# Optimization experiments

Hardware: AMD Instinct MI355X
Metric: run time of the kernel (lower is better)

The kernel has to match this reference:

```python
import jax, jax.numpy as jnp
import numpy as np

B, N, F_IN, H, C = 32768, 12, 128, 4, 64  # batch, nodes/graph, input_dim, heads, hidden_dim
NEG_SLOPE = 0.2  # PyG GATConv default leaky_relu slope


def setup_inputs() -> dict:
    key = jax.random.key(0)
    ks = jax.random.split(key, 16)
    def xavier(k, shape):
        fan_in, fan_out = shape[0], int(np.prod(shape[1:]))
        lim = float(np.sqrt(6.0 / (fan_in + fan_out)))
        return jax.random.uniform(k, shape, jnp.float32, -lim, lim)
    return {
        "node_features": jax.random.normal(ks[0], (B, N, F_IN), jnp.float32),
        "W1": xavier(ks[1], (F_IN, H, C)),
        "a_src1": xavier(ks[2], (H, C)),
        "a_dst1": xavier(ks[3], (H, C)),
        "b1": jnp.zeros((H * C,), jnp.float32),
        "W2": xavier(ks[4], (H * C, 1, C)),
        "a_src2": xavier(ks[5], (1, C)),
        "a_dst2": xavier(ks[6], (1, C)),
        "b2": jnp.zeros((C,), jnp.float32),
        # classifier head: 64 -> 32 -> 1
        "Wc1": xavier(ks[7], (C, C // 2)),
        "bc1": jnp.zeros((C // 2,), jnp.float32),
        "Wc2": xavier(ks[8], (C // 2, 1)),
        "bc2": jnp.zeros((1,), jnp.float32),
    }


def gat_dense(x, W, a_src, a_dst, bias, concat):
    # x: [B, N, F].  Fully-connected graph + self-loops (PyG GATConv default)
    # == dense attention over all N nodes of each graph.
    h = jnp.einsum("bnf,fhc->bnhc", x, W)               # [B,N,H,C]
    e_src = jnp.einsum("bnhc,hc->bnh", h, a_src)         # alpha contrib of source j
    e_dst = jnp.einsum("bnhc,hc->bnh", h, a_dst)         # alpha contrib of target i
    # edge (j -> i): logit = leaky_relu(e_dst[i] + e_src[j])
    logits = jax.nn.leaky_relu(e_dst[:, :, None, :] + e_src[:, None, :, :], NEG_SLOPE)  # [B,i,j,H]
    alpha = jax.nn.softmax(logits, axis=2)               # softmax over neighbors j
    out = jnp.einsum("bijh,bjhc->bihc", alpha, h)        # aggregate
    if concat:
        out = out.reshape(out.shape[0], out.shape[1], -1)
    else:
        out = out.mean(axis=2)
    return out + bias


def reference(node_features, W1, a_src1, a_dst1, b1, W2, a_src2, a_dst2, b2,
              Wc1, bc1, Wc2, bc2):
    # eval mode: dropouts are identity; is_finetune=False so finetune_block skipped
    x = jax.nn.elu(gat_dense(node_features, W1, a_src1, a_dst1, b1, concat=True))   # [B,N,256]
    x = jax.nn.elu(gat_dense(x, W2, a_src2, a_dst2, b2, concat=False))              # [B,N,64]
    g = x.mean(axis=1)                                                              # global_mean_pool -> [B,64]
    hdn = jax.nn.relu(g @ Wc1 + bc1)
    logits = hdn @ Wc2 + bc2                                                        # [B,1]
    return logits
```

## Files before the change

kernel.cpp:

```cpp
#include <hip/hip_runtime.h>
#include <math.h>

typedef __attribute__((ext_vector_type(8))) short bf16x8;
typedef __attribute__((ext_vector_type(4))) float f32x4;

namespace {
constexpr int NN  = 12;
constexpr int FIN = 128;
constexpr int D1  = 256;
constexpr int C2  = 64;
constexpr float SLOPE = 0.2f;

__device__ __forceinline__ unsigned short f2bf(float f) {
    unsigned u = __builtin_bit_cast(unsigned, f);
    u += 0x7FFFu + ((u >> 16) & 1u);
    return (unsigned short)(u >> 16);
}
__device__ __forceinline__ unsigned pktrunc(float lo, float hi) {
    return __builtin_amdgcn_perm(__builtin_bit_cast(unsigned, hi),
                                 __builtin_bit_cast(unsigned, lo), 0x07060302u);
}
__device__ __forceinline__ float elu1(float x) { return x > 0.f ? x : __expf(x) - 1.f; }
__device__ __forceinline__ float lrelu(float x) { return x > 0.f ? x : SLOPE * x; }
}

__global__ void prep_weights(const float* __restrict__ W1, const float* __restrict__ as1,
                             const float* __restrict__ ad1,
                             const float* __restrict__ W2, const float* __restrict__ as2,
                             const float* __restrict__ ad2,
                             unsigned short* __restrict__ wsB1, unsigned short* __restrict__ wsB2) {
    int t = blockIdx.x * 256 + threadIdx.x;
    if (t < 34816) {
        int i = t & 7, l = (t >> 3) & 63, kn = t >> 9;
        int kt = kn / 17, nt = kn % 17;
        int k = kt * 32 + (l >> 4) * 8 + i;
        float v = 0.f;
        if (nt < 16) {
            v = W1[k * 256 + nt * 16 + (l & 15)];
        } else {
            int cc = l & 15;
            if (cc < 4)      for (int c = 0; c < 64; ++c) v += W1[k * 256 + cc * 64 + c] * as1[cc * 64 + c];
            else if (cc < 8) for (int c = 0; c < 64; ++c) v += W1[k * 256 + (cc - 4) * 64 + c] * ad1[(cc - 4) * 64 + c];
        }
        wsB1[t] = f2bf(v);
    } else if (t < 55296) {
        int t2 = t - 34816;
        int i = t2 & 7, l = (t2 >> 3) & 63, kn = t2 >> 9;
        int kt = kn / 5, nt = kn % 5;
        int k = kt * 32 + (l >> 4) * 8 + i;
        float v = 0.f;
        if (nt < 4) {
            v = W2[k * 64 + nt * 16 + (l & 15)];
        } else {
            int cc = l & 15;
            if (cc == 0)      for (int c = 0; c < 64; ++c) v += W2[k * 64 + c] * as2[c];
            else if (cc == 1) for (int c = 0; c < 64; ++c) v += W2[k * 64 + c] * ad2[c];
        }
        wsB2[t2] = f2bf(v);
    }
}

__global__ __launch_bounds__(512, 4) void gat_mfma8(
    const float* __restrict__ x_in,
    const unsigned short* __restrict__ wsB1,
    const unsigned short* __restrict__ wsB2,
    const float* __restrict__ b1, const float* __restrict__ b2,
    const float* __restrict__ Wc1, const float* __restrict__ bc1,
    const float* __restrict__ Wc2, const float* __restrict__ bc2,
    float* __restrict__ out)
{
    __shared__ __align__(16) unsigned char R0[13056];
    __shared__ __align__(16) unsigned char R1[32768];
    __shared__ __align__(16) unsigned char R2[24576];
    __shared__ float eS1[48][4], eD1[48][4];
    __shared__ float eS2[48], eD2[48];
    __shared__ float gpool[4][64];

    const int b = blockIdx.x, t = threadIdx.x;
    const int w = t >> 6, l = t & 63, l15 = l & 15, lq = l >> 4;

    {
        const float4* xs = (const float4*)(x_in + (size_t)b * (4 * NN * FIN));
        #pragma unroll
        for (int it = 0; it < 3; ++it) {
            int q = t + 512 * it;
            float4 v = xs[q];
            int e0 = q << 2, r = e0 >> 7, k = e0 & 127;
            int addr = ((r << 8) + (k << 1)) ^ ((r & 7) << 4);
            *(uint2*)(R0 + addr) = make_uint2(pktrunc(v.x, v.y), pktrunc(v.z, v.w));
        }
        #pragma unroll
        for (int it = 0; it < 3; ++it)
            *(uint4*)(R2 + ((it * 512 + t) << 4)) = make_uint4(0, 0, 0, 0);
        {
            int col = t >> 1, bs = 6 + (t & 1);
            int addr = ((col << 7) + (bs << 4)) ^ ((col & 7) << 4);
            *(uint4*)(R1 + addr) = make_uint4(0, 0, 0, 0);
        }
    }
    __syncthreads();

    {
        const uint4* pb = (const uint4*)wsB1;
        const int h = w >> 1, half = w & 1;
        bf16x8 Bf[2][4];
        #pragma unroll
        for (int ngl = 0; ngl < 2; ++ngl)
            #pragma unroll
            for (int kt = 0; kt < 4; ++kt)
                Bf[ngl][kt] = __builtin_bit_cast(bf16x8, pb[(kt * 17 + (h * 4 + half * 2 + ngl)) * 64 + l]);
        bf16x8 Bfe[4];
        if (w == 0) {
            #pragma unroll
            for (int kt = 0; kt < 4; ++kt)
                Bfe[kt] = __builtin_bit_cast(bf16x8, pb[(kt * 17 + 16) * 64 + l]);
        }
        #pragma unroll
        for (int m = 0; m < 3; ++m) {
            int r = m * 16 + l15, abase = (r << 8) + (lq << 4), swz = (r & 7) << 4;
            bf16x8 Af[4];
            #pragma unroll
            for (int kt = 0; kt < 4; ++kt)
                Af[kt] = *(const bf16x8*)(R0 + ((abase + (kt << 6)) ^ swz));
            f32x4 acc[2];
            #pragma unroll
            for (int ngl = 0; ngl < 2; ++ngl) acc[ngl] = (f32x4){0.f, 0.f, 0.f, 0.f};
            #pragma unroll
            for (int ngl = 0; ngl < 2; ++ngl)
                #pragma unroll
                for (int kt = 0; kt < 4; ++kt)
                    acc[ngl] = __builtin_amdgcn_mfma_f32_16x16x32_bf16(Af[kt], Bf[ngl][kt], acc[ngl], 0, 0, 0);
            int row0 = m * 16 + lq * 4;
            #pragma unroll
            for (int ngl = 0; ngl < 2; ++ngl) {
                int col = h * 64 + (half * 2 + ngl) * 16 + l15;
                int addr = ((col << 7) + (row0 << 1)) ^ ((col & 7) << 4);
                *(uint2*)(R1 + addr) = make_uint2(pktrunc(acc[ngl][0], acc[ngl][1]),
                                                  pktrunc(acc[ngl][2], acc[ngl][3]));
            }
            if (w == 0) {
                f32x4 acce = (f32x4){0.f, 0.f, 0.f, 0.f};
                #pragma unroll
                for (int kt = 0; kt < 4; ++kt)
                    acce = __builtin_amdgcn_mfma_f32_16x16x32_bf16(Af[kt], Bfe[kt], acce, 0, 0, 0);
                if (l15 < 8) {
                    #pragma unroll
                    for (int reg = 0; reg < 4; ++reg) {
                        int row = row0 + reg;
                        if (l15 < 4) eS1[row][l15] = acce[reg];
                        else         eD1[row][l15 - 4] = acce[reg];
                    }
                }
            }
        }
    }
    __syncthreads();

    if (t < 192) {
        int g = t / 48, rem = t % 48, i = rem >> 2, h = rem & 3;
        int rowi = g * 12 + i;
        float edi = eD1[rowi][h];
        float lv[12]; float mx = -1e30f;
        #pragma unroll
        for (int j = 0; j < 12; ++j) {
            float v = lrelu(edi + eS1[g * 12 + j][h]);
            lv[j] = v; mx = fmaxf(mx, v);
        }
        float s = 0.f;
        #pragma unroll
        for (int j = 0; j < 12; ++j) { lv[j] = __expf(lv[j] - mx); s += lv[j]; }
        float inv = 1.f / s;
        unsigned char* base = R2 + h * 6144;
        int rb = rowi << 7, swz = (rowi & 7) << 4, ob = g * 24;
        #pragma unroll
        for (int p = 0; p < 3; ++p) {
            unsigned q0 = (unsigned)f2bf(lv[4*p]   * inv) | ((unsigned)f2bf(lv[4*p+1] * inv) << 16);
            unsigned q1 = (unsigned)f2bf(lv[4*p+2] * inv) | ((unsigned)f2bf(lv[4*p+3] * inv) << 16);
            int addr = (rb + ob + p * 8) ^ swz;
            *(uint2*)(base + addr) = make_uint2(q0, q1);
        }
    }
    __syncthreads();

    {
        const int h = w >> 1, half = w & 1;
        bf16x8 Ba[3][2];
        const unsigned char* ab = R2 + h * 6144;
        #pragma unroll
        for (int nt = 0; nt < 3; ++nt)
            #pragma unroll
            for (int kt = 0; kt < 2; ++kt) {
                int i = nt * 16 + l15;
                Ba[nt][kt] = *(const bf16x8*)(ab + (((i << 7) + (kt << 6) + (lq << 4)) ^ ((i & 7) << 4)));
            }
        __syncthreads();
        #pragma unroll
        for (int mtl = 0; mtl < 2; ++mtl) {
            int mt = half * 2 + mtl;
            int o = h * 64 + mt * 16 + l15;
            bf16x8 Ah[2];
            #pragma unroll
            for (int kt = 0; kt < 2; ++kt)
                Ah[kt] = *(const bf16x8*)(R1 + (((o << 7) + (kt << 6) + (lq << 4)) ^ ((o & 7) << 4)));
            int o0 = h * 64 + mt * 16 + (lq << 2);
            float4 b1v = *(const float4*)(b1 + o0);
            float bb[4] = {b1v.x, b1v.y, b1v.z, b1v.w};
            #pragma unroll
            for (int nt = 0; nt < 3; ++nt) {
                f32x4 acc = (f32x4){0.f, 0.f, 0.f, 0.f};
                #pragma unroll
                for (int kt = 0; kt < 2; ++kt)
                    acc = __builtin_amdgcn_mfma_f32_16x16x32_bf16(Ah[kt], Ba[nt][kt], acc, 0, 0, 0);
                float e0 = elu1(acc[0] + bb[0]), e1 = elu1(acc[1] + bb[1]);
                float e2 = elu1(acc[2] + bb[2]), e3 = elu1(acc[3] + bb[3]);
                int i = nt * 16 + l15;
                int addr = ((i << 9) + (o0 << 1)) ^ ((i & 7) << 4);
                *(uint2*)(R2 + addr) = make_uint2(pktrunc(e0, e1), pktrunc(e2, e3));
            }
        }
    }
    __syncthreads();

    {
        if (t < 128) {
            int col = t >> 1, bs = 6 + (t & 1);
            int addr = ((col << 7) + (bs << 4)) ^ ((col & 7) << 4);
            *(uint4*)(R1 + addr) = make_uint4(0, 0, 0, 0);
        }
        if (t < 192) {
            *(uint4*)(R1 + 8192 + (t << 4)) = make_uint4(0, 0, 0, 0);
            *(uint4*)(R1 + 8192 + ((t + 192) << 4)) = make_uint4(0, 0, 0, 0);
        }
        const uint4* pb2 = (const uint4*)wsB2;
        #pragma unroll
        for (int ui = 0; ui < 2; ++ui) {
            int u = w * 2 + ui;
            if (u < 15) {
                int tile = u / 3, m = u % 3;
                bf16x8 Bg[8];
                #pragma unroll
                for (int kt = 0; kt < 8; ++kt)
                    Bg[kt] = __builtin_bit_cast(bf16x8, pb2[(kt * 5 + tile) * 64 + l]);
                int r = m * 16 + l15, swz = (r & 7) << 4;
                f32x4 acc = (f32x4){0.f, 0.f, 0.f, 0.f};
                #pragma unroll
                for (int kt = 0; kt < 8; ++kt) {
                    int addr = ((r << 9) + (kt << 6) + (lq << 4)) ^ swz;
                    bf16x8 Ax = *(const bf16x8*)(R2 + addr);
                    acc = __builtin_amdgcn_mfma_f32_16x16x32_bf16(Ax, Bg[kt], acc, 0, 0, 0);
                }
                int row0 = m * 16 + lq * 4;
                if (tile < 4) {
                    int col = tile * 16 + l15;
                    int addr = ((col << 7) + (row0 << 1)) ^ ((col & 7) << 4);
                    *(uint2*)(R1 + addr) = make_uint2(pktrunc(acc[0], acc[1]),
                                                      pktrunc(acc[2], acc[3]));
                } else if (l15 < 2) {
                    #pragma unroll
                    for (int reg = 0; reg < 4; ++reg) {
                        int row = row0 + reg;
                        if (l15 == 0) eS2[row] = acc[reg];
                        else          eD2[row] = acc[reg];
                    }
                }
            }
        }
    }
    __syncthreads();

    if (t < 48) {
        int g = t / 12;
        float edi = eD2[t];
        float lv[12]; float mx = -1e30f;
        #pragma unroll
        for (int j = 0; j < 12; ++j) {
            float v = lrelu(edi + eS2[g * 12 + j]);
            lv[j] = v; mx = fmaxf(mx, v);
        }
        float s = 0.f;
        #pragma unroll
        for (int j = 0; j < 12; ++j) { lv[j] = __expf(lv[j] - mx); s += lv[j]; }
        float inv = 1.f / s;
        int rb = t << 7, swz = (t & 7) << 4, ob = g * 24;
        #pragma unroll
        for (int p = 0; p < 3; ++p) {
            unsigned q0 = (unsigned)f2bf(lv[4*p]   * inv) | ((unsigned)f2bf(lv[4*p+1] * inv) << 16);
            unsigned q1 = (unsigned)f2bf(lv[4*p+2] * inv) | ((unsigned)f2bf(lv[4*p+3] * inv) << 16);
            int addr = 8192 + ((rb + ob + p * 8) ^ swz);
            *(uint2*)(R1 + addr) = make_uint2(q0, q1);
        }
    }
    __syncthreads();

    {
        const int mt = w & 3;
        const int nt0 = (w < 4) ? 0 : 2;
        const int ntc = (w < 4) ? 2 : 1;
        int o = mt * 16 + l15;
        bf16x8 Ah2[2];
        #pragma unroll
        for (int kt = 0; kt < 2; ++kt)
            Ah2[kt] = *(const bf16x8*)(R1 + (((o << 7) + (kt << 6) + (lq << 4)) ^ ((o & 7) << 4)));
        int ost = mt * 16 + (lq << 2);
        float4 b2v = *(const float4*)(b2 + ost);
        float bb[4] = {b2v.x, b2v.y, b2v.z, b2v.w};
        for (int ni = 0; ni < ntc; ++ni) {
            int nt = nt0 + ni;
            int i = nt * 16 + l15;
            bf16x8 Ba2[2];
            #pragma unroll
            for (int kt = 0; kt < 2; ++kt)
                Ba2[kt] = *(const bf16x8*)(R1 + 8192 + (((i << 7) + (kt << 6) + (lq << 4)) ^ ((i & 7) << 4)));
            f32x4 acc = (f32x4){0.f, 0.f, 0.f, 0.f};
            #pragma unroll
            for (int kt = 0; kt < 2; ++kt)
                acc = __builtin_amdgcn_mfma_f32_16x16x32_bf16(Ah2[kt], Ba2[kt], acc, 0, 0, 0);
            #pragma unroll
            for (int reg = 0; reg < 4; ++reg)
                *(float*)(R0 + (ost + reg) * 200 + (i << 2)) = elu1(acc[reg] + bb[reg]);
        }
    }
    __syncthreads();

    if (t < 256) {
        int o = t & 63, g = t >> 6;
        const unsigned char* row = R0 + o * 200 + g * 48;
        float s = 0.f;
        #pragma unroll
        for (int p = 0; p < 6; ++p) {
            float2 v = *(const float2*)(row + p * 8);
            s += v.x + v.y;
        }
        gpool[g][o] = s * (1.0f / 12.0f);
    }
    __syncthreads();

    if (t < 128) {
        int g = t >> 5, nr = t & 31;
        float acc = bc1[nr];
        #pragma unroll
        for (int cc = 0; cc < 64; ++cc)
            acc = fmaf(gpool[g][cc], Wc1[cc * 32 + nr], acc);
        float val = fmaxf(acc, 0.f) * Wc2[nr];
        #pragma unroll
        for (int msk = 1; msk < 32; msk <<= 1) val += __shfl_xor(val, msk);
        if (nr == 0) out[b * 4 + g] = val + bc2[0];
    }
}

__global__ __launch_bounds__(256, 4) void gat_fused_f32(
    const float* __restrict__ x_in, const float* __restrict__ W1,
    const float* __restrict__ a_src1, const float* __restrict__ a_dst1,
    const float* __restrict__ b1, const float* __restrict__ W2,
    const float* __restrict__ a_src2, const float* __restrict__ a_dst2,
    const float* __restrict__ b2, const float* __restrict__ Wc1,
    const float* __restrict__ bc1, const float* __restrict__ Wc2,
    const float* __restrict__ bc2, float* __restrict__ out)
{
    __shared__ union {
        float x_l[NN][FIN];
        struct { float h2[NN][C2]; float x3[NN][C2]; } s2;
    } u;
    __shared__ float h1s[NN][D1];
    __shared__ float x2s[NN][D1];
    __shared__ float alpha1[NN][NN][4];
    __shared__ float e_s1[NN][4], e_d1[NN][4];
    __shared__ float e_s2[NN], e_d2[NN];
    __shared__ float alpha2[NN][NN];
    __shared__ float gph[C2];
    __shared__ float hdn[32];

    const int b = blockIdx.x, t = threadIdx.x;
    const float* xb = x_in + (size_t)b * (NN * FIN);
    for (int i = t; i < NN * FIN; i += 256) (&u.x_l[0][0])[i] = xb[i];
    __syncthreads();
    {
        const int o0 = (t & 127) * 2, n0 = (t >> 7) * 6;
        float acc[6][2];
        #pragma unroll
        for (int i = 0; i < 6; ++i) { acc[i][0] = 0.f; acc[i][1] = 0.f; }
        for (int f = 0; f < FIN; f += 4) {
            float4 xv[6];
            #pragma unroll
            for (int i = 0; i < 6; ++i) xv[i] = *(const float4*)&u.x_l[n0 + i][f];
            #pragma unroll
            for (int k = 0; k < 4; ++k) {
                const float2 wv = *(const float2*)&W1[(f + k) * D1 + o0];
                #pragma unroll
                for (int i = 0; i < 6; ++i) {
                    const float xs = ((const float*)&xv[i])[k];
                    acc[i][0] = fmaf(xs, wv.x, acc[i][0]);
                    acc[i][1] = fmaf(xs, wv.y, acc[i][1]);
                }
            }
        }
        #pragma unroll
        for (int i = 0; i < 6; ++i) { h1s[n0+i][o0] = acc[i][0]; h1s[n0+i][o0+1] = acc[i][1]; }
    }
    __syncthreads();
    if (t < NN * 4) {
        const int n = t >> 2, h = t & 3;
        float es = 0.f, ed = 0.f;
        for (int c = 0; c < 64; ++c) {
            const float v = h1s[n][h * 64 + c];
            es = fmaf(v, a_src1[h * 64 + c], es);
            ed = fmaf(v, a_dst1[h * 64 + c], ed);
        }
        e_s1[n][h] = es; e_d1[n][h] = ed;
    }
    __syncthreads();
    if (t < NN * 4) {
        const int i = t >> 2, h = t & 3;
        const float edi = e_d1[i][h];
        float lv[NN]; float m = -1e30f;
        #pragma unroll
        for (int j = 0; j < NN; ++j) {
            float v = edi + e_s1[j][h]; v = v > 0.f ? v : SLOPE * v;
            lv[j] = v; m = fmaxf(m, v);
        }
        float s = 0.f;
        #pragma unroll
        for (int j = 0; j < NN; ++j) { lv[j] = __expf(lv[j] - m); s += lv[j]; }
        const float inv = 1.f / s;
        #pragma unroll
        for (int j = 0; j < NN; ++j) alpha1[i][j][h] = lv[j] * inv;
    }
    __syncthreads();
    {
        const int o = t, h = o >> 6;
        const float bo = b1[o];
        float v[NN];
        #pragma unroll
        for (int j = 0; j < NN; ++j) v[j] = h1s[j][o];
        #pragma unroll
        for (int i = 0; i < NN; ++i) {
            float acc = 0.f;
            #pragma unroll
            for (int j = 0; j < NN; ++j) acc = fmaf(alpha1[i][j][h], v[j], acc);
            x2s[i][o] = acc + bo > 0.f ? acc + bo : expm1f(acc + bo);
        }
    }
    __syncthreads();
    {
        const int c = t & 63, n0 = (t >> 6) * 3;
        float acc[3] = {0.f, 0.f, 0.f};
        for (int f = 0; f < D1; f += 4) {
            float4 xv[3];
            #pragma unroll
            for (int i = 0; i < 3; ++i) xv[i] = *(const float4*)&x2s[n0 + i][f];
            #pragma unroll
            for (int k = 0; k < 4; ++k) {
                const float wv = W2[(f + k) * C2 + c];
                #pragma unroll
                for (int i = 0; i < 3; ++i) acc[i] = fmaf(((const float*)&xv[i])[k], wv, acc[i]);
            }
        }
        #pragma unroll
        for (int i = 0; i < 3; ++i) u.s2.h2[n0 + i][c] = acc[i];
    }
    __syncthreads();
    if (t < NN) {
        float es = 0.f, ed = 0.f;
        for (int c = 0; c < 64; c += 4) {
            const float4 v  = *(const float4*)&u.s2.h2[t][c];
            const float4 as = *(const float4*)&a_src2[c];
            const float4 ad = *(const float4*)&a_dst2[c];
            es += v.x*as.x + v.y*as.y + v.z*as.z + v.w*as.w;
            ed += v.x*ad.x + v.y*ad.y + v.z*ad.z + v.w*ad.w;
        }
        e_s2[t] = es; e_d2[t] = ed;
    }
    __syncthreads();
    if (t < NN) {
        const float edi = e_d2[t];
        float lv[NN]; float m = -1e30f;
        #pragma unroll
        for (int j = 0; j < NN; ++j) {
            float v = edi + e_s2[j]; v = v > 0.f ? v : SLOPE * v;
            lv[j] = v; m = fmaxf(m, v);
        }
        float s = 0.f;
        #pragma unroll
        for (int j = 0; j < NN; ++j) { lv[j] = __expf(lv[j] - m); s += lv[j]; }
        const float inv = 1.f / s;
        #pragma unroll
        for (int j = 0; j < NN; ++j) alpha2[t][j] = lv[j] * inv;
    }
    __syncthreads();
    {
        const int c = t & 63, i0 = (t >> 6) * 3;
        float v[NN];
        #pragma unroll
        for (int j = 0; j < NN; ++j) v[j] = u.s2.h2[j][c];
        const float bc = b2[c];
        #pragma unroll
        for (int ii = 0; ii < 3; ++ii) {
            const int i = i0 + ii;
            float acc = 0.f;
            #pragma unroll
            for (int j = 0; j < NN; ++j) acc = fmaf(alpha2[i][j], v[j], acc);
            u.s2.x3[i][c] = acc + bc > 0.f ? acc + bc : expm1f(acc + bc);
        }
    }
    __syncthreads();
    if (t < C2) {
        float s = 0.f;
        #pragma unroll
        for (int i = 0; i < NN; ++i) s += u.s2.x3[i][t];
        gph[t] = s * (1.0f / NN);
    }
    __syncthreads();
    if (t < 32) {
        float acc = bc1[t];
        for (int c = 0; c < C2; ++c) acc = fmaf(gph[c], Wc1[c * 32 + t], acc);
        hdn[t] = fmaxf(acc, 0.f);
    }
    __syncthreads();
    if (t == 0) {
        float acc = bc2[0];
        #pragma unroll
        for (int k = 0; k < 32; ++k) acc = fmaf(hdn[k], Wc2[k], acc);
        out[b] = acc;
    }
}

extern "C" void kernel_launch(void* const* d_in, const int* in_sizes, int n_in,
                              void* d_out, int out_size, void* d_ws, size_t ws_size,
                              hipStream_t stream) {
    const float* x   = (const float*)d_in[0];
    const float* W1  = (const float*)d_in[1];
    const float* as1 = (const float*)d_in[2];
    const float* ad1 = (const float*)d_in[3];
    const float* b1  = (const float*)d_in[4];
    const float* W2  = (const float*)d_in[5];
    const float* as2 = (const float*)d_in[6];
    const float* ad2 = (const float*)d_in[7];
    const float* b2  = (const float*)d_in[8];
    const float* Wc1 = (const float*)d_in[9];
    const float* bc1 = (const float*)d_in[10];
    const float* Wc2 = (const float*)d_in[11];
    const float* bc2 = (const float*)d_in[12];
    float* out = (float*)d_out;

    const int B = in_sizes[0] / (NN * FIN);

    if (ws_size >= 110592 && (B % 4) == 0) {
        unsigned short* wsB1 = (unsigned short*)d_ws;
        unsigned short* wsB2 = wsB1 + 34816;
        prep_weights<<<216, 256, 0, stream>>>(W1, as1, ad1, W2, as2, ad2, wsB1, wsB2);
        gat_mfma8<<<B / 4, 512, 0, stream>>>(x, wsB1, wsB2, b1, b2, Wc1, bc1, Wc2, bc2, out);
    } else {
        gat_fused_f32<<<B, 256, 0, stream>>>(x, W1, as1, ad1, b1, W2, as2, ad2, b2,
                                             Wc1, bc1, Wc2, bc2, out);
    }
}
```

Before: 145.6 us.

## Keep layer-1 projection in registers via lane shuffles and shrink LDS for occupancy

The layer-1 projection results stay in registers as packed bf16 and are rebuilt into MFMA A-fragments with cross-lane shuffles, instead of being written to and read back from a transposed LDS buffer. This shrinks the shared-memory footprint: R1 drops from 32 KB to 14 KB, R0 loses its padding, and gpool moves into an existing buffer. The launch bound is raised to 6 blocks per CU. The aim is to cut LDS traffic and raise occupancy, at the cost of more VGPR pressure from the held fragments and extra shuffle instructions.

```diff
diff --git a/kernel.cpp b/kernel.cpp
--- a/kernel.cpp
+++ b/kernel.cpp
@@ -60,7 +60,7 @@
     }
 }
 
-__global__ __launch_bounds__(512, 4) void gat_mfma8(
+__global__ __launch_bounds__(512, 6) void gat_mfma10(
     const float* __restrict__ x_in,
     const unsigned short* __restrict__ wsB1,
     const unsigned short* __restrict__ wsB2,
@@ -69,15 +69,15 @@
     const float* __restrict__ Wc2, const float* __restrict__ bc2,
     float* __restrict__ out)
 {
-    __shared__ __align__(16) unsigned char R0[13056];
-    __shared__ __align__(16) unsigned char R1[32768];
+    __shared__ __align__(16) unsigned char R0[12288];
+    __shared__ __align__(16) unsigned char R1[14336];
     __shared__ __align__(16) unsigned char R2[24576];
     __shared__ float eS1[48][4], eD1[48][4];
     __shared__ float eS2[48], eD2[48];
-    __shared__ float gpool[4][64];
 
     const int b = blockIdx.x, t = threadIdx.x;
     const int w = t >> 6, l = t & 63, l15 = l & 15, lq = l >> 4;
+    const int h = w >> 1, half = w & 1;
 
     {
         const float4* xs = (const float4*)(x_in + (size_t)b * (4 * NN * FIN));
@@ -92,17 +92,12 @@
         #pragma unroll
         for (int it = 0; it < 3; ++it)
             *(uint4*)(R2 + ((it * 512 + t) << 4)) = make_uint4(0, 0, 0, 0);
-        {
-            int col = t >> 1, bs = 6 + (t & 1);
-            int addr = ((col << 7) + (bs << 4)) ^ ((col & 7) << 4);
-            *(uint4*)(R1 + addr) = make_uint4(0, 0, 0, 0);
-        }
-    }
-    __syncthreads();
-
+    }
+    __syncthreads();
+
+    unsigned qp[3][2][2];
     {
         const uint4* pb = (const uint4*)wsB1;
-        const int h = w >> 1, half = w & 1;
         bf16x8 Bf[2][4];
         #pragma unroll
         for (int ngl = 0; ngl < 2; ++ngl)
@@ -130,13 +125,10 @@
                 #pragma unroll
                 for (int kt = 0; kt < 4; ++kt)
                     acc[ngl] = __builtin_amdgcn_mfma_f32_16x16x32_bf16(Af[kt], Bf[ngl][kt], acc[ngl], 0, 0, 0);
-            int row0 = m * 16 + lq * 4;
             #pragma unroll
             for (int ngl = 0; ngl < 2; ++ngl) {
-                int col = h * 64 + (half * 2 + ngl) * 16 + l15;
-                int addr = ((col << 7) + (row0 << 1)) ^ ((col & 7) << 4);
-                *(uint2*)(R1 + addr) = make_uint2(pktrunc(acc[ngl][0], acc[ngl][1]),
-                                                  pktrunc(acc[ngl][2], acc[ngl][3]));
+                qp[m][ngl][0] = pktrunc(acc[ngl][0], acc[ngl][1]);
+                qp[m][ngl][1] = pktrunc(acc[ngl][2], acc[ngl][3]);
             }
             if (w == 0) {
                 f32x4 acce = (f32x4){0.f, 0.f, 0.f, 0.f};
@@ -144,6 +136,7 @@
                 for (int kt = 0; kt < 4; ++kt)
                     acce = __builtin_amdgcn_mfma_f32_16x16x32_bf16(Af[kt], Bfe[kt], acce, 0, 0, 0);
                 if (l15 < 8) {
+                    int row0 = m * 16 + lq * 4;
                     #pragma unroll
                     for (int reg = 0; reg < 4; ++reg) {
                         int row = row0 + reg;
@@ -157,20 +150,20 @@
     __syncthreads();
 
     if (t < 192) {
-        int g = t / 48, rem = t % 48, i = rem >> 2, h = rem & 3;
+        int g = t / 48, rem = t % 48, i = rem >> 2, hh = rem & 3;
         int rowi = g * 12 + i;
-        float edi = eD1[rowi][h];
+        float edi = eD1[rowi][hh];
         float lv[12]; float mx = -1e30f;
         #pragma unroll
         for (int j = 0; j < 12; ++j) {
-            float v = lrelu(edi + eS1[g * 12 + j][h]);
+            float v = lrelu(edi + eS1[g * 12 + j][hh]);
             lv[j] = v; mx = fmaxf(mx, v);
         }
         float s = 0.f;
         #pragma unroll
         for (int j = 0; j < 12; ++j) { lv[j] = __expf(lv[j] - mx); s += lv[j]; }
         float inv = 1.f / s;
-        unsigned char* base = R2 + h * 6144;
+        unsigned char* base = R2 + hh * 6144;
         int rb = rowi << 7, swz = (rowi & 7) << 4, ob = g * 24;
         #pragma unroll
         for (int p = 0; p < 3; ++p) {
@@ -183,7 +176,6 @@
     __syncthreads();
 
     {
-        const int h = w >> 1, half = w & 1;
         bf16x8 Ba[3][2];
         const unsigned char* ab = R2 + h * 6144;
         #pragma unroll
@@ -194,23 +186,36 @@
                 Ba[nt][kt] = *(const bf16x8*)(ab + (((i << 7) + (kt << 6) + (lq << 4)) ^ ((i & 7) << 4)));
             }
         __syncthreads();
+        const int sA = (((lq * 2) & 3) << 4) + l15;
+        const int sB = sA + 16;
+        const bool lo = (lq < 2);
         #pragma unroll
         for (int mtl = 0; mtl < 2; ++mtl) {
             int mt = half * 2 + mtl;
-            int o = h * 64 + mt * 16 + l15;
-            bf16x8 Ah[2];
-            #pragma unroll
-            for (int kt = 0; kt < 2; ++kt)
-                Ah[kt] = *(const bf16x8*)(R1 + (((o << 7) + (kt << 6) + (lq << 4)) ^ ((o & 7) << 4)));
+            unsigned a0 = (unsigned)__shfl((int)qp[0][mtl][0], sA);
+            unsigned a1 = (unsigned)__shfl((int)qp[0][mtl][1], sA);
+            unsigned a2 = (unsigned)__shfl((int)qp[0][mtl][0], sB);
+            unsigned a3 = (unsigned)__shfl((int)qp[0][mtl][1], sB);
+            unsigned b0 = (unsigned)__shfl((int)qp[1][mtl][0], sA);
+            unsigned b1r = (unsigned)__shfl((int)qp[1][mtl][1], sA);
+            unsigned b2 = (unsigned)__shfl((int)qp[1][mtl][0], sB);
+            unsigned b3 = (unsigned)__shfl((int)qp[1][mtl][1], sB);
+            uint4 f0 = make_uint4(lo ? a0 : b0, lo ? a1 : b1r, lo ? a2 : b2, lo ? a3 : b3);
+            unsigned c0 = (unsigned)__shfl((int)qp[2][mtl][0], sA);
+            unsigned c1 = (unsigned)__shfl((int)qp[2][mtl][1], sA);
+            unsigned c2 = (unsigned)__shfl((int)qp[2][mtl][0], sB);
+            unsigned c3 = (unsigned)__shfl((int)qp[2][mtl][1], sB);
+            uint4 f1 = lo ? make_uint4(c0, c1, c2, c3) : make_uint4(0, 0, 0, 0);
+            bf16x8 Ah0 = __builtin_bit_cast(bf16x8, f0);
+            bf16x8 Ah1 = __builtin_bit_cast(bf16x8, f1);
             int o0 = h * 64 + mt * 16 + (lq << 2);
             float4 b1v = *(const float4*)(b1 + o0);
             float bb[4] = {b1v.x, b1v.y, b1v.z, b1v.w};
             #pragma unroll
             for (int nt = 0; nt < 3; ++nt) {
                 f32x4 acc = (f32x4){0.f, 0.f, 0.f, 0.f};
-                #pragma unroll
-                for (int kt = 0; kt < 2; ++kt)
-                    acc = __builtin_amdgcn_mfma_f32_16x16x32_bf16(Ah[kt], Ba[nt][kt], acc, 0, 0, 0);
+                acc = __builtin_amdgcn_mfma_f32_16x16x32_bf16(Ah0, Ba[nt][0], acc, 0, 0, 0);
+                acc = __builtin_amdgcn_mfma_f32_16x16x32_bf16(Ah1, Ba[nt][1], acc, 0, 0, 0);
                 float e0 = elu1(acc[0] + bb[0]), e1 = elu1(acc[1] + bb[1]);
                 float e2 = elu1(acc[2] + bb[2]), e3 = elu1(acc[3] + bb[3]);
                 int i = nt * 16 + l15;
@@ -317,30 +322,31 @@
                 acc = __builtin_amdgcn_mfma_f32_16x16x32_bf16(Ah2[kt], Ba2[kt], acc, 0, 0, 0);
             #pragma unroll
             for (int reg = 0; reg < 4; ++reg)
-                *(float*)(R0 + (ost + reg) * 200 + (i << 2)) = elu1(acc[reg] + bb[reg]);
+                *(float*)(R0 + (ost + reg) * 192 + (i << 2)) = elu1(acc[reg] + bb[reg]);
         }
     }
     __syncthreads();
 
     if (t < 256) {
         int o = t & 63, g = t >> 6;
-        const unsigned char* row = R0 + o * 200 + g * 48;
+        const unsigned char* row = R0 + o * 192 + g * 48;
         float s = 0.f;
         #pragma unroll
         for (int p = 0; p < 6; ++p) {
             float2 v = *(const float2*)(row + p * 8);
             s += v.x + v.y;
         }
-        gpool[g][o] = s * (1.0f / 12.0f);
+        ((float*)(R1 + 8192))[g * 64 + o] = s * (1.0f / 12.0f);
     }
     __syncthreads();
 
     if (t < 128) {
         int g = t >> 5, nr = t & 31;
+        const float* gp = (const float*)(R1 + 8192);
         float acc = bc1[nr];
         #pragma unroll
         for (int cc = 0; cc < 64; ++cc)
-            acc = fmaf(gpool[g][cc], Wc1[cc * 32 + nr], acc);
+            acc = fmaf(gp[g * 64 + cc], Wc1[cc * 32 + nr], acc);
         float val = fmaxf(acc, 0.f) * Wc2[nr];
         #pragma unroll
         for (int msk = 1; msk < 32; msk <<= 1) val += __shfl_xor(val, msk);
@@ -548,7 +554,7 @@
         unsigned short* wsB1 = (unsigned short*)d_ws;
         unsigned short* wsB2 = wsB1 + 34816;
         prep_weights<<<216, 256, 0, stream>>>(W1, as1, ad1, W2, as2, ad2, wsB1, wsB2);
-        gat_mfma8<<<B / 4, 512, 0, stream>>>(x, wsB1, wsB2, b1, b2, Wc1, bc1, Wc2, bc2, out);
+        gat_mfma10<<<B / 4, 512, 0, stream>>>(x, wsB1, wsB2, b1, b2, Wc1, bc1, Wc2, bc2, out);
     } else {
         gat_fused_f32<<<B, 256, 0, stream>>>(x, W1, as1, ad1, b1, W2, as2, ad2, b2,
                                              Wc1, bc1, Wc2, bc2, out);
```

Result: no change. 147.2 us (+1.2%).
